# Performance work log

Hardware: AMD Instinct MI355X
Metric: run time of the kernel (lower is better)

Reference implementation:

```python
import jax, jax.numpy as jnp
import numpy as np

HEADS = 4
DIM_HEAD = 32


def setup_inputs() -> dict:
    key = jax.random.key(0)
    k1, k2, k3, k4 = jax.random.split(key, 4)
    dim = 128
    hidden = HEADS * DIM_HEAD  # 128
    x = jax.random.normal(k1, (32, dim, 64, 64), dtype=jnp.float32)
    w_qkv = jax.random.normal(k2, (3 * hidden, dim), dtype=jnp.float32) * (1.0 / np.sqrt(dim))
    w_out = jax.random.normal(k3, (dim, hidden), dtype=jnp.float32) * (1.0 / np.sqrt(hidden))
    b_out = jax.random.normal(k4, (dim,), dtype=jnp.float32) * 0.01
    return {"x": x, "w_qkv": w_qkv, "w_out": w_out, "b_out": b_out}


def reference(x, w_qkv, w_out, b_out):
    b, c, h, w = x.shape
    n = h * w
    # 1x1 conv (no bias) == channel matmul
    qkv = jnp.einsum('oc,bchw->bohw', w_qkv, x)  # [b, 3*heads*dh, h, w]
    qkv = qkv.reshape(b, 3, HEADS, DIM_HEAD, n)
    q, k, v = qkv[:, 0], qkv[:, 1], qkv[:, 2]  # each [b, heads, dh, n]
    k = jax.nn.softmax(k, axis=-1)  # softmax over spatial positions
    context = jnp.einsum('bhdn,bhen->bhde', k, v)  # [b, heads, dh, dh]
    out = jnp.einsum('bhde,bhdn->bhen', context, q)  # [b, heads, dh, n]
    out = out.reshape(b, HEADS * DIM_HEAD, h, w)
    # 1x1 conv with bias
    return jnp.einsum('oc,bchw->bohw', w_out, out) + b_out[None, :, None, None]
```

## Files before the change

### kernel.cpp

```cpp
#include <hip/hip_runtime.h>
#include <hip/hip_bf16.h>
#include <math.h>

#define BATCH 32
#define CDIM  128
#define NTOT  4096
#define NCH   16
#define CHN   256
#define TN    64

typedef __attribute__((ext_vector_type(4))) float f32x4;
typedef __attribute__((ext_vector_type(8))) short s16x8;

#define PC_OFF  0
#define PC_SIZE (BATCH * 4 * NCH * 32 * 32)
#define PS_OFF  (PC_OFF + PC_SIZE)
#define PS_SIZE (BATCH * 4 * NCH * 32)
#define WBF_OFF (PS_OFF + PS_SIZE)
#define MBF_OFF (WBF_OFF + 24576)
#define CTX_OFF (MBF_OFF + 262144)

static __device__ __forceinline__ unsigned short f2bf(float f) {
    return __builtin_bit_cast(unsigned short, __float2bfloat16(f));
}
static __device__ __forceinline__ unsigned int pack2(float a, float b) {
    return (unsigned int)f2bf(a) | ((unsigned int)f2bf(b) << 16);
}
static __device__ __forceinline__ s16x8 ld_frag_lds(const unsigned int* xsd, int d0) {
    int4 t;
    t.x = (int)xsd[d0]; t.y = (int)xsd[d0 + 1];
    t.z = (int)xsd[d0 + 2]; t.w = (int)xsd[d0 + 3];
    return __builtin_bit_cast(s16x8, t);
}

static __device__ __forceinline__ void stage_xT(const float* __restrict__ xc,
                                                unsigned int* __restrict__ xsd,
                                                int tid) {
    const int m  = tid & 15;
    const int cg = tid >> 4;
#pragma unroll
    for (int p = 0; p < 4; ++p) {
        const int c = 2 * cg + 32 * p;
        const f32x4 a0 = *reinterpret_cast<const f32x4*>(xc + (size_t)c * NTOT + 4 * m);
        const f32x4 a1 = *reinterpret_cast<const f32x4*>(xc + (size_t)(c + 1) * NTOT + 4 * m);
#pragma unroll
        for (int jj = 0; jj < 4; ++jj)
            xsd[(4 * m + jj) * 65 + (c >> 1)] = pack2(a0[jj], a1[jj]);
    }
}

__global__ void k0_wcvt(const float* __restrict__ wqkv, float* __restrict__ ws) {
    const int i = blockIdx.x * 256 + threadIdx.x;
    unsigned short* wbf = (unsigned short*)(ws + WBF_OFF);
    if (i < 384 * CDIM) wbf[i] = f2bf(wqkv[i]);
}

__global__ __launch_bounds__(256, 2)
void k1_ctx(const float* __restrict__ x, const unsigned short* __restrict__ wbf,
            float* __restrict__ ws) {
    __shared__ __attribute__((aligned(16))) unsigned short xsT[64 * 130];
    __shared__ __attribute__((aligned(16))) unsigned short ekv[8][32][72];

    const int j = blockIdx.x, b = blockIdx.y;
    const int tid = threadIdx.x;
    const int l = tid & 63;
    const int w = tid >> 6;
    const int m = l & 15, hq = l >> 4;

    s16x8 afr[4][4];
#pragma unroll
    for (int tm = 0; tm < 4; ++tm)
#pragma unroll
        for (int kt = 0; kt < 4; ++kt)
            afr[tm][kt] = *reinterpret_cast<const s16x8*>(
                wbf + (size_t)(CDIM + 64 * w + 16 * tm + m) * CDIM + 32 * kt + 8 * hq);

    f32x4 cacc[2][2] = {};
    float sacc[4][4] = {};
    const float* xc = x + (size_t)b * CDIM * NTOT + j * CHN;
    unsigned int* xsd = (unsigned int*)xsT;

    for (int it = 0; it < CHN / TN; ++it) {
        stage_xT(xc + it * TN, xsd, tid);
        __syncthreads();

        f32x4 acc[4][4] = {};
#pragma unroll
        for (int kt = 0; kt < 4; ++kt) {
#pragma unroll
            for (int tn = 0; tn < 4; ++tn) {
                const s16x8 bfr = ld_frag_lds(xsd, (16 * tn + m) * 65 + 16 * kt + 4 * hq);
#pragma unroll
                for (int tm = 0; tm < 4; ++tm)
                    acc[tm][tn] = __builtin_amdgcn_mfma_f32_16x16x32_bf16(
                        afr[tm][kt], bfr, acc[tm][tn], 0, 0, 0);
            }
        }

        if (w < 2) {
#pragma unroll
            for (int tm = 0; tm < 4; ++tm)
#pragma unroll
                for (int tn = 0; tn < 4; ++tn)
#pragma unroll
                    for (int r = 0; r < 4; ++r) {
                        const int dg = 64 * w + 16 * tm + 4 * hq + r;
                        const float e = __expf(acc[tm][tn][r]);
                        sacc[tm][r] += e;
                        ekv[dg >> 5][dg & 31][16 * tn + m] = f2bf(e);
                    }
        } else {
#pragma unroll
            for (int tm = 0; tm < 4; ++tm)
#pragma unroll
                for (int tn = 0; tn < 4; ++tn)
#pragma unroll
                    for (int r = 0; r < 4; ++r) {
                        const int eg = 64 * (w - 2) + 16 * tm + 4 * hq + r;
                        ekv[4 + (eg >> 5)][eg & 31][16 * tn + m] = f2bf(acc[tm][tn][r]);
                    }
        }
        __syncthreads();

#pragma unroll
        for (int kt = 0; kt < 2; ++kt) {
            s16x8 va[2], eb[2];
#pragma unroll
            for (int t = 0; t < 2; ++t) {
                va[t] = *reinterpret_cast<const s16x8*>(
                    &ekv[4 + w][16 * t + m][32 * kt + 8 * hq]);
                eb[t] = *reinterpret_cast<const s16x8*>(
                    &ekv[w][16 * t + m][32 * kt + 8 * hq]);
            }
#pragma unroll
            for (int tm = 0; tm < 2; ++tm)
#pragma unroll
                for (int tn = 0; tn < 2; ++tn)
                    cacc[tm][tn] = __builtin_amdgcn_mfma_f32_16x16x32_bf16(
                        va[tm], eb[tn], cacc[tm][tn], 0, 0, 0);
        }
        __syncthreads();
    }

    float* pc = ws + PC_OFF + (size_t)((b * 4 + w) * NCH + j) * 1024;
#pragma unroll
    for (int tm = 0; tm < 2; ++tm)
#pragma unroll
        for (int tn = 0; tn < 2; ++tn)
#pragma unroll
            for (int r = 0; r < 4; ++r)
                pc[(16 * tm + 4 * hq + r) * 32 + 16 * tn + m] = cacc[tm][tn][r];

    if (w < 2) {
#pragma unroll
        for (int tm = 0; tm < 4; ++tm)
#pragma unroll
            for (int r = 0; r < 4; ++r) {
                float s = sacc[tm][r];
                s += __shfl_xor(s, 1);
                s += __shfl_xor(s, 2);
                s += __shfl_xor(s, 4);
                s += __shfl_xor(s, 8);
                if (m == 0) {
                    const int dg = 64 * w + 16 * tm + 4 * hq + r;
                    ws[PS_OFF + (size_t)((b * 4 + (dg >> 5)) * NCH + j) * 32 + (dg & 31)] = s;
                }
            }
    }
}

__global__ __launch_bounds__(256)
void k2a_ctx(float* __restrict__ ws) {
    const int bh = blockIdx.x;
    const int tid = threadIdx.x;
    __shared__ float stotS[32];
    if (tid < 32) {
        float s = 0.f;
        for (int j = 0; j < NCH; ++j)
            s += ws[PS_OFF + (size_t)(bh * NCH + j) * 32 + tid];
        stotS[tid] = s;
    }
    __syncthreads();
#pragma unroll
    for (int k = 0; k < 4; ++k) {
        const int idx = tid + 256 * k;
        float c = 0.f;
        for (int j = 0; j < NCH; ++j)
            c += ws[PC_OFF + (size_t)(bh * NCH + j) * 1024 + idx];
        ws[CTX_OFF + (size_t)bh * 1024 + idx] = c / stotS[idx & 31];
    }
}

__global__ __launch_bounds__(256)
void k2b_buildM(const float* __restrict__ wout, float* __restrict__ ws) {
    const int oq = blockIdx.x;
    const int b  = blockIdx.y;
    const int tid = threadIdx.x;

    __shared__ __attribute__((aligned(16))) float smA[8704];
    __shared__ float G[32][133];
    float* ctxs  = smA;
    float* wouts = smA + 4224;
    unsigned int* wqs = (unsigned int*)smA;

#pragma unroll
    for (int k = 0; k < 16; ++k) {
        const int fid = tid + 256 * k;
        const int h = fid >> 10, rem = fid & 1023;
        const int e = rem >> 5, d = rem & 31;
        ctxs[(h * 32 + d) * 33 + e] = ws[CTX_OFF + (size_t)b * 4096 + fid];
    }
#pragma unroll
    for (int k = 0; k < 16; ++k) {
        const int fid = tid + 256 * k;
        const int o = fid >> 7, c = fid & 127;
        wouts[o * 133 + c] = wout[(size_t)(oq * 32 + o) * CDIM + c];
    }
    __syncthreads();

    {
        const int o2 = tid & 31;
        const int g8 = tid >> 5;
#pragma unroll
        for (int i = 0; i < 16; ++i) {
            const int hd = g8 * 16 + i;
            const int h = hd >> 5;
            float acc = 0.f;
#pragma unroll
            for (int e = 0; e < 32; ++e)
                acc = fmaf(wouts[o2 * 133 + h * 32 + e], ctxs[hd * 33 + e], acc);
            G[o2][hd] = acc;
        }
    }
    __syncthreads();

    {
        const unsigned int* wbfu = (const unsigned int*)(ws + WBF_OFF);
#pragma unroll
        for (int k = 0; k < 32; ++k) {
            const int fid = tid + 256 * k;
            const int hd = fid >> 6, cd = fid & 63;
            wqs[hd * 68 + cd] = wbfu[fid];
        }
    }
    __syncthreads();

    {
        const int o3 = tid >> 3;
        const int c0 = tid & 7;
        float Macc[16];
#pragma unroll
        for (int i = 0; i < 16; ++i) Macc[i] = 0.f;
        for (int hd = 0; hd < 128; ++hd) {
            const float gv = G[o3][hd];
            const uint4 w0 = *reinterpret_cast<const uint4*>(&wqs[hd * 68 + c0 * 8]);
            const uint4 w1 = *reinterpret_cast<const uint4*>(&wqs[hd * 68 + c0 * 8 + 4]);
            const unsigned int dw[8] = {w0.x, w0.y, w0.z, w0.w, w1.x, w1.y, w1.z, w1.w};
#pragma unroll
            for (int q = 0; q < 8; ++q) {
                const float lo = __builtin_bit_cast(float, dw[q] << 16);
                const float hi = __builtin_bit_cast(float, dw[q] & 0xffff0000u);
                Macc[2 * q]     = fmaf(gv, lo, Macc[2 * q]);
                Macc[2 * q + 1] = fmaf(gv, hi, Macc[2 * q + 1]);
            }
        }
        unsigned int* mpd = (unsigned int*)((unsigned short*)(ws + MBF_OFF) +
                                            (size_t)b * CDIM * CDIM) +
                            (oq * 32 + o3) * 64 + c0 * 8;
        uint4 s0, s1;
        s0.x = pack2(Macc[0], Macc[1]);   s0.y = pack2(Macc[2], Macc[3]);
        s0.z = pack2(Macc[4], Macc[5]);   s0.w = pack2(Macc[6], Macc[7]);
        s1.x = pack2(Macc[8], Macc[9]);   s1.y = pack2(Macc[10], Macc[11]);
        s1.z = pack2(Macc[12], Macc[13]); s1.w = pack2(Macc[14], Macc[15]);
        *reinterpret_cast<uint4*>(mpd) = s0;
        *reinterpret_cast<uint4*>(mpd + 4) = s1;
    }
}

__global__ __launch_bounds__(256)
void k3_final(const float* __restrict__ x, const float* __restrict__ bout,
              const float* __restrict__ ws, float* __restrict__ out) {
    __shared__ __attribute__((aligned(16))) unsigned short xsT[64 * 130];

    const int j = blockIdx.x, b = blockIdx.y;
    const int tid = threadIdx.x, l = tid & 63, w = tid >> 6;
    const int m = l & 15, hq = l >> 4;

    const unsigned short* mbf =
        (const unsigned short*)(ws + MBF_OFF) + (size_t)b * CDIM * CDIM;
    s16x8 afr[2][4];
#pragma unroll
    for (int tm = 0; tm < 2; ++tm)
#pragma unroll
        for (int kt = 0; kt < 4; ++kt)
            afr[tm][kt] = *reinterpret_cast<const s16x8*>(
                mbf + (size_t)(32 * w + 16 * tm + m) * CDIM + 32 * kt + 8 * hq);
    float bias[2][4];
#pragma unroll
    for (int tm = 0; tm < 2; ++tm)
#pragma unroll
        for (int r = 0; r < 4; ++r)
            bias[tm][r] = bout[32 * w + 16 * tm + 4 * hq + r];

    unsigned int* xsd = (unsigned int*)xsT;
    const float* xc = x + (size_t)b * CDIM * NTOT + j * CHN;
    float* oc = out + (size_t)b * CDIM * NTOT + j * CHN;

    for (int it = 0; it < CHN / TN; ++it) {
        stage_xT(xc + it * TN, xsd, tid);
        __syncthreads();
        f32x4 acc[2][4] = {};
#pragma unroll
        for (int kt = 0; kt < 4; ++kt) {
#pragma unroll
            for (int tn = 0; tn < 4; ++tn) {
                const s16x8 bfr = ld_frag_lds(xsd, (16 * tn + m) * 65 + 16 * kt + 4 * hq);
#pragma unroll
                for (int tm = 0; tm < 2; ++tm)
                    acc[tm][tn] = __builtin_amdgcn_mfma_f32_16x16x32_bf16(
                        afr[tm][kt], bfr, acc[tm][tn], 0, 0, 0);
            }
        }
#pragma unroll
        for (int tm = 0; tm < 2; ++tm)
#pragma unroll
            for (int tn = 0; tn < 4; ++tn)
#pragma unroll
                for (int r = 0; r < 4; ++r)
                    oc[(size_t)(32 * w + 16 * tm + 4 * hq + r) * NTOT +
                       it * TN + 16 * tn + m] = acc[tm][tn][r] + bias[tm][r];
        __syncthreads();
    }
}

extern "C" void kernel_launch(void* const* d_in, const int* in_sizes, int n_in,
                              void* d_out, int out_size, void* d_ws, size_t ws_size,
                              hipStream_t stream) {
    const float* x    = (const float*)d_in[0];
    const float* wqkv = (const float*)d_in[1];
    const float* wout = (const float*)d_in[2];
    const float* bout = (const float*)d_in[3];
    float* out = (float*)d_out;
    float* ws  = (float*)d_ws;

    k0_wcvt<<<192, 256, 0, stream>>>(wqkv, ws);
    k1_ctx<<<dim3(NCH, BATCH), 256, 0, stream>>>(
        x, (const unsigned short*)(ws + WBF_OFF), ws);
    k2a_ctx<<<BATCH * 4, 256, 0, stream>>>(ws);
    k2b_buildM<<<dim3(4, BATCH), 256, 0, stream>>>(wout, ws);
    k3_final<<<dim3(NCH, BATCH), 256, 0, stream>>>(x, bout, ws, out);
}
```

Before: 79.49 us.

## Cache bf16 transposed x from k1 for k3, fold weight conversion and ctx reduction

Drops the separate weight-conversion kernel by converting w_qkv to bf16 inline in k1 and k2. Merges the ctx reduction kernel into buildM, which cuts two launches. When workspace is large enough, k1 writes its LDS-staged bf16 transposed x tiles, XOR-swizzled, to workspace so k3 can load them with straight vector copies and swizzled 16-byte LDS reads. This halves the x bytes k3 reads and removes its transpose and pack work, at the cost of an extra 32 MB write in k1 and redundant weight conversion per block.

```diff
diff --git a/kernel.cpp b/kernel.cpp
--- a/kernel.cpp
+++ b/kernel.cpp
@@ -16,9 +16,11 @@
 #define PC_SIZE (BATCH * 4 * NCH * 32 * 32)
 #define PS_OFF  (PC_OFF + PC_SIZE)
 #define PS_SIZE (BATCH * 4 * NCH * 32)
-#define WBF_OFF (PS_OFF + PS_SIZE)
-#define MBF_OFF (WBF_OFF + 24576)
-#define CTX_OFF (MBF_OFF + 262144)
+#define MBF_OFF (PS_OFF + PS_SIZE)
+#define MBF_SIZE (BATCH * CDIM * CDIM / 2)
+#define XBT_OFF (MBF_OFF + MBF_SIZE)
+#define XBT_SIZE (BATCH * CDIM * NTOT / 2)
+#define NEED_BYTES ((size_t)(XBT_OFF + XBT_SIZE) * 4)
 
 static __device__ __forceinline__ unsigned short f2bf(float f) {
     return __builtin_bit_cast(unsigned short, __float2bfloat16(f));
@@ -49,14 +51,9 @@
     }
 }
 
-__global__ void k0_wcvt(const float* __restrict__ wqkv, float* __restrict__ ws) {
-    const int i = blockIdx.x * 256 + threadIdx.x;
-    unsigned short* wbf = (unsigned short*)(ws + WBF_OFF);
-    if (i < 384 * CDIM) wbf[i] = f2bf(wqkv[i]);
-}
-
+template <bool XBT>
 __global__ __launch_bounds__(256, 2)
-void k1_ctx(const float* __restrict__ x, const unsigned short* __restrict__ wbf,
+void k1_ctx(const float* __restrict__ x, const float* __restrict__ wqkv,
             float* __restrict__ ws) {
     __shared__ __attribute__((aligned(16))) unsigned short xsT[64 * 130];
     __shared__ __attribute__((aligned(16))) unsigned short ekv[8][32][72];
@@ -71,9 +68,16 @@
 #pragma unroll
     for (int tm = 0; tm < 4; ++tm)
 #pragma unroll
-        for (int kt = 0; kt < 4; ++kt)
-            afr[tm][kt] = *reinterpret_cast<const s16x8*>(
-                wbf + (size_t)(CDIM + 64 * w + 16 * tm + m) * CDIM + 32 * kt + 8 * hq);
+        for (int kt = 0; kt < 4; ++kt) {
+            const float* wr = wqkv +
+                (size_t)(CDIM + 64 * w + 16 * tm + m) * CDIM + 32 * kt + 8 * hq;
+            const f32x4 u0 = *reinterpret_cast<const f32x4*>(wr);
+            const f32x4 u1 = *reinterpret_cast<const f32x4*>(wr + 4);
+            int4 t4;
+            t4.x = (int)pack2(u0[0], u0[1]); t4.y = (int)pack2(u0[2], u0[3]);
+            t4.z = (int)pack2(u1[0], u1[1]); t4.w = (int)pack2(u1[2], u1[3]);
+            afr[tm][kt] = __builtin_bit_cast(s16x8, t4);
+        }
 
     f32x4 cacc[2][2] = {};
     float sacc[4][4] = {};
@@ -83,6 +87,21 @@
     for (int it = 0; it < CHN / TN; ++it) {
         stage_xT(xc + it * TN, xsd, tid);
         __syncthreads();
+
+        if constexpr (XBT) {
+            unsigned int* tb = (unsigned int*)(ws + XBT_OFF) +
+                               ((size_t)(b * NCH + j) * 4 + it) * 4096;
+            const int n = tid >> 2, qt = tid & 3;
+#pragma unroll
+            for (int p = 0; p < 4; ++p) {
+                const int cdl = 16 * p + 4 * qt;
+                const int src = n * 65 + (cdl ^ ((n & 7) << 2));
+                uint4 v;
+                v.x = xsd[src]; v.y = xsd[src + 1];
+                v.z = xsd[src + 2]; v.w = xsd[src + 3];
+                *reinterpret_cast<uint4*>(tb + (size_t)n * 64 + cdl) = v;
+            }
+        }
 
         f32x4 acc[4][4] = {};
 #pragma unroll
@@ -170,45 +189,37 @@
 }
 
 __global__ __launch_bounds__(256)
-void k2a_ctx(float* __restrict__ ws) {
-    const int bh = blockIdx.x;
-    const int tid = threadIdx.x;
-    __shared__ float stotS[32];
-    if (tid < 32) {
-        float s = 0.f;
-        for (int j = 0; j < NCH; ++j)
-            s += ws[PS_OFF + (size_t)(bh * NCH + j) * 32 + tid];
-        stotS[tid] = s;
-    }
-    __syncthreads();
-#pragma unroll
-    for (int k = 0; k < 4; ++k) {
-        const int idx = tid + 256 * k;
-        float c = 0.f;
-        for (int j = 0; j < NCH; ++j)
-            c += ws[PC_OFF + (size_t)(bh * NCH + j) * 1024 + idx];
-        ws[CTX_OFF + (size_t)bh * 1024 + idx] = c / stotS[idx & 31];
-    }
-}
-
-__global__ __launch_bounds__(256)
-void k2b_buildM(const float* __restrict__ wout, float* __restrict__ ws) {
+void k2_buildM(const float* __restrict__ wqkv, const float* __restrict__ wout,
+               float* __restrict__ ws) {
     const int oq = blockIdx.x;
     const int b  = blockIdx.y;
     const int tid = threadIdx.x;
 
     __shared__ __attribute__((aligned(16))) float smA[8704];
     __shared__ float G[32][133];
+    __shared__ float stotS[128];
     float* ctxs  = smA;
     float* wouts = smA + 4224;
     unsigned int* wqs = (unsigned int*)smA;
+
+    if (tid < 128) {
+        const int h = tid >> 5, d = tid & 31;
+        float s = 0.f;
+        for (int j = 0; j < NCH; ++j)
+            s += ws[PS_OFF + (size_t)((b * 4 + h) * NCH + j) * 32 + d];
+        stotS[tid] = s;
+    }
+    __syncthreads();
 
 #pragma unroll
     for (int k = 0; k < 16; ++k) {
         const int fid = tid + 256 * k;
         const int h = fid >> 10, rem = fid & 1023;
         const int e = rem >> 5, d = rem & 31;
-        ctxs[(h * 32 + d) * 33 + e] = ws[CTX_OFF + (size_t)b * 4096 + fid];
+        float c = 0.f;
+        for (int j = 0; j < NCH; ++j)
+            c += ws[PC_OFF + (size_t)((b * 4 + h) * NCH + j) * 1024 + rem];
+        ctxs[(h * 32 + d) * 33 + e] = c / stotS[h * 32 + d];
     }
 #pragma unroll
     for (int k = 0; k < 16; ++k) {
@@ -235,12 +246,13 @@
     __syncthreads();
 
     {
-        const unsigned int* wbfu = (const unsigned int*)(ws + WBF_OFF);
 #pragma unroll
         for (int k = 0; k < 32; ++k) {
             const int fid = tid + 256 * k;
             const int hd = fid >> 6, cd = fid & 63;
-            wqs[hd * 68 + cd] = wbfu[fid];
+            const float2 wv =
+                *reinterpret_cast<const float2*>(wqkv + (size_t)hd * CDIM + 2 * cd);
+            wqs[hd * 68 + cd] = pack2(wv.x, wv.y);
         }
     }
     __syncthreads();
@@ -277,6 +289,7 @@
     }
 }
 
+template <bool XBT>
 __global__ __launch_bounds__(256)
 void k3_final(const float* __restrict__ x, const float* __restrict__ bout,
               const float* __restrict__ ws, float* __restrict__ out) {
@@ -307,14 +320,34 @@
     float* oc = out + (size_t)b * CDIM * NTOT + j * CHN;
 
     for (int it = 0; it < CHN / TN; ++it) {
-        stage_xT(xc + it * TN, xsd, tid);
-        __syncthreads();
+        if constexpr (XBT) {
+            const unsigned int* tb = (const unsigned int*)(ws + XBT_OFF) +
+                                     ((size_t)(b * NCH + j) * 4 + it) * 4096;
+#pragma unroll
+            for (int rep = 0; rep < 4; ++rep) {
+                const int dw = rep * 1024 + tid * 4;
+                *reinterpret_cast<uint4*>(&xsd[dw]) =
+                    *reinterpret_cast<const uint4*>(tb + dw);
+            }
+        } else {
+            stage_xT(xc + it * TN, xsd, tid);
+        }
+        __syncthreads();
+
         f32x4 acc[2][4] = {};
 #pragma unroll
         for (int kt = 0; kt < 4; ++kt) {
 #pragma unroll
             for (int tn = 0; tn < 4; ++tn) {
-                const s16x8 bfr = ld_frag_lds(xsd, (16 * tn + m) * 65 + 16 * kt + 4 * hq);
+                const int nl = 16 * tn + m;
+                s16x8 bfr;
+                if constexpr (XBT) {
+                    const int idx = nl * 64 + ((16 * kt + 4 * hq) ^ ((nl & 7) << 2));
+                    bfr = __builtin_bit_cast(
+                        s16x8, *reinterpret_cast<const int4*>(&xsd[idx]));
+                } else {
+                    bfr = ld_frag_lds(xsd, nl * 65 + 16 * kt + 4 * hq);
+                }
 #pragma unroll
                 for (int tm = 0; tm < 2; ++tm)
                     acc[tm][tn] = __builtin_amdgcn_mfma_f32_16x16x32_bf16(
@@ -343,10 +376,17 @@
     float* out = (float*)d_out;
     float* ws  = (float*)d_ws;
 
-    k0_wcvt<<<192, 256, 0, stream>>>(wqkv, ws);
-    k1_ctx<<<dim3(NCH, BATCH), 256, 0, stream>>>(
-        x, (const unsigned short*)(ws + WBF_OFF), ws);
-    k2a_ctx<<<BATCH * 4, 256, 0, stream>>>(ws);
-    k2b_buildM<<<dim3(4, BATCH), 256, 0, stream>>>(wout, ws);
-    k3_final<<<dim3(NCH, BATCH), 256, 0, stream>>>(x, bout, ws, out);
-}
+    const bool xbt = ws_size >= NEED_BYTES;
+
+    if (xbt)
+        k1_ctx<true><<<dim3(NCH, BATCH), 256, 0, stream>>>(x, wqkv, ws);
+    else
+        k1_ctx<false><<<dim3(NCH, BATCH), 256, 0, stream>>>(x, wqkv, ws);
+
+    k2_buildM<<<dim3(4, BATCH), 256, 0, stream>>>(wqkv, wout, ws);
+
+    if (xbt)
+        k3_final<true><<<dim3(NCH, BATCH), 256, 0, stream>>>(x, bout, ws, out);
+    else
+        k3_final<false><<<dim3(NCH, BATCH), 256, 0, stream>>>(x, bout, ws, out);
+}
```

Result: no change. 78.05 us (-1.8%).
